# Performance work log

Hardware: AMD Instinct MI355X
Metric: run time of the kernel (lower is better)

The kernel has to match this reference:

```python
import jax, jax.numpy as jnp
import numpy as np

# 5x5 binomial Gaussian kernel, normalized by 256
_K = jnp.array([[1., 4., 6., 4., 1.],
                [4., 16., 24., 16., 4.],
                [6., 24., 36., 24., 6.],
                [4., 16., 24., 16., 4.],
                [1., 4., 6., 4., 1.]], dtype=jnp.float32) / 256.0


def _gauss_conv(img, kernel):
    # depthwise 5x5 conv with reflect padding 2 (same spatial size)
    C = img.shape[1]
    p = jnp.pad(img, ((0, 0), (0, 0), (2, 2), (2, 2)), mode='reflect')
    return jax.lax.conv_general_dilated(
        p, kernel, window_strides=(1, 1), padding='VALID',
        dimension_numbers=('NCHW', 'OIHW', 'NCHW'),
        feature_group_count=C)


def _lap_pyramid(img, kernel, max_levels=5):
    pyr = []
    cur = img
    for _ in range(max_levels):  # fixed small loop over pyramid levels
        H, W = cur.shape[2], cur.shape[3]
        cur = cur[:, :, :H - H % 2, :W - W % 2]  # crop to even size
        down = _gauss_conv(cur, kernel)[:, :, ::2, ::2]
        up = jnp.zeros(cur.shape, cur.dtype).at[:, :, ::2, ::2].set(down * 4.0)
        up = _gauss_conv(up, kernel)
        pyr.append(cur - up)
        cur = down
    return pyr


def setup_inputs() -> dict:
    key = jax.random.key(0)
    k1, k2 = jax.random.split(key)
    predict = jax.random.uniform(k1, (16, 3, 512, 512), dtype=jnp.float32)
    target = jax.random.uniform(k2, (16, 3, 512, 512), dtype=jnp.float32)
    return {"predict": predict, "target": target}


def reference(predict, target):
    C = predict.shape[1]
    kernel = jnp.tile(_K.astype(predict.dtype)[None, None], (C, 1, 1, 1))  # [C,1,5,5]
    pyr_p = _lap_pyramid(predict, kernel, 5)
    pyr_t = _lap_pyramid(target, kernel, 5)
    weights = (1.0, 2.0, 4.0, 8.0, 16.0)
    loss = jnp.asarray(0.0, predict.dtype)
    for w, a, b in zip(weights, pyr_p, pyr_t):
        loss = loss + w * jnp.mean(jnp.abs(a - b))  # F.l1_loss (mean reduction)
    return loss
```

## Files before the change

kernel.cpp:

```cpp
#include <hip/hip_runtime.h>


__device__ __forceinline__ int reflect_i(int m, int S) {
    if (m < 0) m = -m;
    if (m >= S) m = 2 * S - 2 - m;
    return m;
}

__device__ __forceinline__ void wg_barrier() {
    asm volatile("s_waitcnt lgkmcnt(0)" ::: "memory");
    __builtin_amdgcn_s_barrier();
}

#define WAITVM(N) asm volatile("s_waitcnt vmcnt(" #N ")" ::: "memory")
#define WAITLGKM0 asm volatile("s_waitcnt lgkmcnt(0)" ::: "memory")

__device__ __forceinline__ void gld16(const void* g, void* l) {
    __builtin_amdgcn_global_load_lds(
        (const __attribute__((address_space(1))) void*)g,
        (__attribute__((address_space(3))) void*)l, 16, 0, 0);
}

template <int CPL>
__device__ __forceinline__ int swz(int B) {
    if constexpr (CPL == 4) return B ^ (((B >> 7) & 7) << 4);
    else return B;
}

template <int S, int ISL0, int DH>
__global__ __launch_bounds__(64)
void pyr_kernel(const float* __restrict__ a, const float* __restrict__ b,
                float* __restrict__ dwn, float* __restrict__ acc, float scale) {
    constexpr int D = S / 2;
    constexpr int CPL = S / 128;
    constexpr int W = 2 * CPL + 3;
    constexpr int ROWB = (CPL == 1) ? 1024 : S * 4;
    constexpr int NRING = 8;

    __shared__ float4 ringmem[(NRING * ROWB * (ISL0 ? 2 : 1)) / 16];
    char* ra = (char*)ringmem;
    char* rb = ra + NRING * ROWB;

    const int lane = threadIdx.x;
    const int bid = blockIdx.x;
    constexpr int NRS = D / DH;
    const int rs = bid % NRS;
    const int n = bid / NRS;
    const int R0 = rs * DH;
    const size_t gbase = (size_t)n * S * S;

    auto stage_row = [&](int s) {
        int gr = reflect_i(2 * R0 - 4 + s, S);
        const char* ga = (const char*)(a + gbase + (size_t)gr * S);
        char* la = ra + (s & 7) * ROWB;
        if constexpr (CPL == 4) {
            gld16(ga + swz<CPL>(16 * lane), la);
            gld16(ga + swz<CPL>(16 * lane + 1024), la + 1024);
        } else if constexpr (CPL == 2) {
            gld16(ga + 16 * lane, la);
        } else {
            gld16(ga + 16 * (lane & 31), la);
        }
        if constexpr (ISL0) {
            const char* gb = (const char*)(b + gbase + (size_t)gr * S);
            char* lb = rb + (s & 7) * ROWB;
            gld16(gb + swz<CPL>(16 * lane), lb);
            gld16(gb + swz<CPL>(16 * lane + 1024), lb + 1024);
        }
    };

    auto read_win = [&](int s, float* w) {
        const char* pa = ra + (s & 7) * ROWB;
        if constexpr (CPL == 4) {
            int bl = 32 * lane;
            float2 lo = *(const float2*)(pa + swz<CPL>(lane ? bl - 8 : 0));
            float4 m0 = *(const float4*)(pa + swz<CPL>(bl));
            float4 m1 = *(const float4*)(pa + swz<CPL>(bl + 16));
            float hi = *(const float*)(pa + swz<CPL>(lane == 63 ? 2032 : bl + 32));
            w[0]=lo.x; w[1]=lo.y; w[2]=m0.x; w[3]=m0.y; w[4]=m0.z; w[5]=m0.w;
            w[6]=m1.x; w[7]=m1.y; w[8]=m1.z; w[9]=m1.w; w[10]=hi;
            if constexpr (ISL0) {
                const char* pb = rb + (s & 7) * ROWB;
                float2 l2 = *(const float2*)(pb + swz<CPL>(lane ? bl - 8 : 0));
                float4 t0 = *(const float4*)(pb + swz<CPL>(bl));
                float4 t1 = *(const float4*)(pb + swz<CPL>(bl + 16));
                float h2 = *(const float*)(pb + swz<CPL>(lane == 63 ? 2032 : bl + 32));
                w[0]-=l2.x; w[1]-=l2.y; w[2]-=t0.x; w[3]-=t0.y; w[4]-=t0.z;
                w[5]-=t0.w; w[6]-=t1.x; w[7]-=t1.y; w[8]-=t1.z; w[9]-=t1.w; w[10]-=h2;
            }
        } else if constexpr (CPL == 2) {
            int bl = 16 * lane;
            float2 lo = *(const float2*)(pa + (lane ? bl - 8 : 0));
            float4 m0 = *(const float4*)(pa + bl);
            float hi = *(const float*)(pa + (lane == 63 ? 1008 : bl + 16));
            w[0]=lo.x; w[1]=lo.y; w[2]=m0.x; w[3]=m0.y; w[4]=m0.z; w[5]=m0.w; w[6]=hi;
        } else {
            int bl = 8 * lane;
            float2 lo = *(const float2*)(pa + (lane ? bl - 8 : 0));
            float2 m0 = *(const float2*)(pa + bl);
            float hi = *(const float*)(pa + (lane == 63 ? 496 : bl + 8));
            w[0]=lo.x; w[1]=lo.y; w[2]=m0.x; w[3]=m0.y; w[4]=hi;
        }
        if (lane == 0)  { w[0] = w[4]; w[1] = w[3]; }
        if (lane == 63) { w[W - 1] = w[W - 3]; }
    };

    auto read_cur = [&](int s, float* c) {
        const char* pa = ra + (s & 7) * ROWB;
        if constexpr (CPL == 4) {
            int bl = 32 * lane;
            float4 x = *(const float4*)(pa + swz<CPL>(bl));
            float4 y = *(const float4*)(pa + swz<CPL>(bl + 16));
            c[0]=x.x; c[1]=x.y; c[2]=x.z; c[3]=x.w; c[4]=y.x; c[5]=y.y; c[6]=y.z; c[7]=y.w;
            if constexpr (ISL0) {
                const char* pb = rb + (s & 7) * ROWB;
                float4 u = *(const float4*)(pb + swz<CPL>(bl));
                float4 v = *(const float4*)(pb + swz<CPL>(bl + 16));
                c[0]-=u.x; c[1]-=u.y; c[2]-=u.z; c[3]-=u.w;
                c[4]-=v.x; c[5]-=v.y; c[6]-=v.z; c[7]-=v.w;
            }
        } else if constexpr (CPL == 2) {
            float4 x = *(const float4*)(pa + 16 * lane);
            c[0]=x.x; c[1]=x.y; c[2]=x.z; c[3]=x.w;
        } else {
            float2 x = *(const float2*)(pa + 8 * lane);
            c[0]=x.x; c[1]=x.y;
        }
    };

    auto hof = [&](const float* w, float* h) {
        #pragma unroll
        for (int j = 0; j < CPL; j++)
            h[j] = w[2*j] + 4.f*w[2*j+1] + 6.f*w[2*j+2] + 4.f*w[2*j+3] + w[2*j+4];
    };

    #pragma unroll
    for (int s = 0; s < 8; ++s) stage_row(s);
    if constexpr (CPL == 4) { WAITVM(20); } else { WAITVM(5); }

    float hA[CPL], hB[CPL], hC[CPL], hD[CPL], hE[CPL];
    {
        float w[W];
        read_win(0, w); hof(w, hA);
        read_win(1, w); hof(w, hB);
        read_win(2, w); hof(w, hC);
    }
    float ex0[CPL] = {}, ex1[CPL] = {}, ex2[CPL], ox0[CPL] = {}, ox1[CPL] = {}, ox2[CPL];
    float sum = 0.f;
    float* dbase = dwn + (size_t)n * D * D;

    #pragma unroll
    for (int it = 0; it <= DH + 1; ++it) {
        const int m = R0 - 1 + it;
        if (it <= DH) {
            if constexpr (CPL == 4) { WAITVM(12); } else { WAITVM(3); }
        } else {
            WAITVM(0);
        }
        {
            float w[W];
            read_win(2 * it + 3, w); hof(w, hD);
            read_win(2 * it + 4, w); hof(w, hE);
        }
        float d[CPL], dl[CPL], dr[CPL];
        #pragma unroll
        for (int j = 0; j < CPL; j++)
            d[j] = (hA[j] + 4.f*hB[j] + 6.f*hC[j] + 4.f*hD[j] + hE[j]) * (1.f / 256.f);
        float dli = __shfl_up(d[CPL - 1], 1, 64);
        float dri = __shfl_down(d[0], 1, 64);
        dl[0] = (lane == 0) ? ((CPL > 1) ? d[1] : dri) : dli;
        #pragma unroll
        for (int j = 1; j < CPL; j++) dl[j] = d[j - 1];
        dr[CPL - 1] = (lane == 63) ? d[CPL - 1] : dri;
        #pragma unroll
        for (int j = 0; j < CPL - 1; j++) dr[j] = d[j + 1];
        #pragma unroll
        for (int j = 0; j < CPL; j++) {
            ex2[j] = 0.125f * (dl[j] + 6.f * d[j] + dr[j]);
            ox2[j] = 0.5f * (d[j] + dr[j]);
        }

        if (it >= 1 && it <= DH) {
            char* dst = (char*)(dbase + (size_t)m * D + CPL * lane);
            if constexpr (CPL == 4)      *(float4*)dst = make_float4(d[0], d[1], d[2], d[3]);
            else if constexpr (CPL == 2) *(float2*)dst = make_float2(d[0], d[1]);
            else                         *(float*)dst = d[0];
        }

        if (it >= 2) {
            const int me = m - 1;
            float cA[2 * CPL], cB[2 * CPL];
            read_cur(2 * it, cA);
            read_cur(2 * it + 1, cB);
            #pragma unroll
            for (int j = 0; j < CPL; j++) {
                float eA = (me == 0) ? ex2[j] : ex0[j];
                float oA = (me == 0) ? ox2[j] : ox0[j];
                float eC = (me == D - 1) ? ex1[j] : ex2[j];
                float oC = (me == D - 1) ? ox1[j] : ox2[j];
                float uee = 0.125f * (eA + 6.f * ex1[j] + eC);
                float ueo = 0.125f * (oA + 6.f * ox1[j] + oC);
                float uoe = 0.5f * (ex1[j] + eC);
                float uoo = 0.5f * (ox1[j] + oC);
                sum += fabsf(cA[2*j] - uee) + fabsf(cA[2*j+1] - ueo)
                     + fabsf(cB[2*j] - uoe) + fabsf(cB[2*j+1] - uoo);
            }
        }

        #pragma unroll
        for (int j = 0; j < CPL; j++) {
            ex0[j] = ex1[j]; ex1[j] = ex2[j];
            ox0[j] = ox1[j]; ox1[j] = ox2[j];
            hA[j] = hC[j]; hB[j] = hD[j]; hC[j] = hE[j];
        }

        if (it <= DH - 1) {
            WAITLGKM0;
            stage_row(8 + 2 * it);
            stage_row(9 + 2 * it);
        }
    }

    #pragma unroll
    for (int o = 32; o > 0; o >>= 1) sum += __shfl_down(sum, o, 64);
    if (lane == 0) atomicAdd(&acc[bid & 63], sum * scale);
}

__device__ float level_in_lds(const float* cur, float* h, float* dn,
                              int S, int tid, int nt) {
    const int D = S >> 1;
    for (int i = tid; i < S * D; i += nt) {
        int r = i / D, xh = i % D;
        int c0 = reflect_i(2 * xh - 2, S), c1 = reflect_i(2 * xh - 1, S);
        int c3 = 2 * xh + 1, c4 = reflect_i(2 * xh + 2, S);
        const float* row = cur + r * S;
        h[i] = row[c0] + 4.f * row[c1] + 6.f * row[2 * xh] + 4.f * row[c3] + row[c4];
    }
    wg_barrier();
    for (int i = tid; i < D * D; i += nt) {
        int yh = i / D, xh = i % D;
        int r0 = reflect_i(2 * yh - 2, S), r1 = reflect_i(2 * yh - 1, S);
        int r3 = 2 * yh + 1, r4 = reflect_i(2 * yh + 2, S);
        dn[i] = (h[r0 * D + xh] + 4.f * h[r1 * D + xh] + 6.f * h[2 * yh * D + xh]
               + 4.f * h[r3 * D + xh] + h[r4 * D + xh]) * (1.f / 256.f);
    }
    wg_barrier();
    float sum = 0.f;
    for (int i = tid; i < D * D; i += nt) {
        int yh2 = i / D, q = i % D;
        int rm = (yh2 == 0) ? 1 : yh2 - 1;
        int rp = (yh2 == D - 1) ? D - 1 : yh2 + 1;
        int cm = (q == 0) ? 1 : q - 1;
        int cp = (q == D - 1) ? D - 1 : q + 1;
        float A00 = dn[rm * D + cm], A01 = dn[rm * D + q], A02 = dn[rm * D + cp];
        float A10 = dn[yh2 * D + cm], A11 = dn[yh2 * D + q], A12 = dn[yh2 * D + cp];
        float A20 = dn[rp * D + cm], A21 = dn[rp * D + q], A22 = dn[rp * D + cp];
        float ex0 = (A00 + 6.f * A01 + A02) * 0.125f;
        float ex1 = (A10 + 6.f * A11 + A12) * 0.125f;
        float ex2 = (A20 + 6.f * A21 + A22) * 0.125f;
        float ox0 = (A01 + A02) * 0.5f;
        float ox1 = (A11 + A12) * 0.5f;
        float ox2 = (A21 + A22) * 0.5f;
        float uee = (ex0 + 6.f * ex1 + ex2) * 0.125f;
        float ueo = (ox0 + 6.f * ox1 + ox2) * 0.125f;
        float uoe = (ex1 + ex2) * 0.5f;
        float uoo = (ox1 + ox2) * 0.5f;
        const float* c0 = cur + (2 * yh2) * S + 2 * q;
        sum += fabsf(c0[0] - uee) + fabsf(c0[1] - ueo)
             + fabsf(c0[S] - uoe) + fabsf(c0[S + 1] - uoo);
    }
    wg_barrier();
    return sum;
}

__global__ __launch_bounds__(256)
void tail_kernel(const float* __restrict__ d2, float* __restrict__ acc,
                 float s3, float s4) {
    __shared__ float cur[64 * 64];
    __shared__ float hbuf[64 * 32];
    __shared__ float dn3[32 * 32];
    __shared__ float dn4[16 * 16];
    int n = blockIdx.x, tid = threadIdx.x;
    const float4* src = (const float4*)(d2 + (size_t)n * 64 * 64);
    for (int i = tid; i < 64 * 16; i += 256) ((float4*)cur)[i] = src[i];
    wg_barrier();
    float sum = level_in_lds(cur, hbuf, dn3, 64, tid, 256) * s3;
    sum += level_in_lds(dn3, hbuf, dn4, 32, tid, 256) * s4;
    #pragma unroll
    for (int o = 32; o > 0; o >>= 1) sum += __shfl_down(sum, o, 64);
    __shared__ float s[4];
    int lane = tid & 63, w = tid >> 6;
    if (lane == 0) s[w] = sum;
    wg_barrier();
    if (tid == 0) atomicAdd(&acc[n & 63], s[0] + s[1] + s[2] + s[3]);
}

__global__ void finish_kernel(const float* __restrict__ acc, float* __restrict__ out) {
    float v = acc[threadIdx.x];
    #pragma unroll
    for (int o = 32; o > 0; o >>= 1) v += __shfl_down(v, o, 64);
    if (threadIdx.x == 0) out[0] = v;
}

extern "C" void kernel_launch(void* const* d_in, const int* in_sizes, int n_in,
                              void* d_out, int out_size, void* d_ws, size_t ws_size,
                              hipStream_t stream) {
    const float* p = (const float*)d_in[0];
    const float* t = (const float*)d_in[1];
    float* out = (float*)d_out;
    float* acc = (float*)d_ws;
    float* dn0 = acc + 64;
    float* dn1 = dn0 + (size_t)48 * 256 * 256;
    float* dn2 = dn1 + (size_t)48 * 128 * 128;

    hipMemsetAsync(acc, 0, 64 * sizeof(float), stream);

    const int N = 48;

    pyr_kernel<512, 1, 16><<<48 * 16, 64, 0, stream>>>(
        p, t, dn0, acc, 1.f / (float)(N * 512 * 512));
    pyr_kernel<256, 0, 8><<<48 * 16, 64, 0, stream>>>(
        dn0, nullptr, dn1, acc, 2.f / (float)(N * 256 * 256));
    pyr_kernel<128, 0, 4><<<48 * 16, 64, 0, stream>>>(
        dn1, nullptr, dn2, acc, 4.f / (float)(N * 128 * 128));
    tail_kernel<<<N, 256, 0, stream>>>(dn2, acc,
                                       8.f / (float)(N * 64 * 64),
                                       16.f / (float)(N * 32 * 32));
    finish_kernel<<<1, 64, 0, stream>>>(acc, out);
}
```

Baseline: 62.68 us.

## Pack four independent wave strips per block with a smaller LDS ring and register-reused rows

Result: slower. 67.85 us (+8.3%).

```diff
diff --git a/kernel.cpp b/kernel.cpp
--- a/kernel.cpp
+++ b/kernel.cpp
@@ -12,8 +12,16 @@
     __builtin_amdgcn_s_barrier();
 }
 
-#define WAITVM(N) asm volatile("s_waitcnt vmcnt(" #N ")" ::: "memory")
-#define WAITLGKM0 asm volatile("s_waitcnt lgkmcnt(0)" ::: "memory")
+#define LGKM0 asm volatile("s_waitcnt lgkmcnt(0)" ::: "memory")
+
+template <int N>
+__device__ __forceinline__ void wait_vm() {
+    if constexpr (N == 0)      asm volatile("s_waitcnt vmcnt(0)" ::: "memory");
+    else if constexpr (N == 1) asm volatile("s_waitcnt vmcnt(1)" ::: "memory");
+    else if constexpr (N == 2) asm volatile("s_waitcnt vmcnt(2)" ::: "memory");
+    else if constexpr (N == 4) asm volatile("s_waitcnt vmcnt(4)" ::: "memory");
+    else if constexpr (N == 8) asm volatile("s_waitcnt vmcnt(8)" ::: "memory");
+}
 
 __device__ __forceinline__ void gld16(const void* g, void* l) {
     __builtin_amdgcn_global_load_lds(
@@ -21,41 +29,38 @@
         (__attribute__((address_space(3))) void*)l, 16, 0, 0);
 }
 
-template <int CPL>
-__device__ __forceinline__ int swz(int B) {
-    if constexpr (CPL == 4) return B ^ (((B >> 7) & 7) << 4);
-    else return B;
-}
+__device__ __forceinline__ int swz4(int B) { return B ^ (((B >> 7) & 7) << 4); }
 
 template <int S, int ISL0, int DH>
-__global__ __launch_bounds__(64)
+__global__ __launch_bounds__(256, 2)
 void pyr_kernel(const float* __restrict__ a, const float* __restrict__ b,
                 float* __restrict__ dwn, float* __restrict__ acc, float scale) {
     constexpr int D = S / 2;
     constexpr int CPL = S / 128;
     constexpr int W = 2 * CPL + 3;
-    constexpr int ROWB = (CPL == 1) ? 1024 : S * 4;
-    constexpr int NRING = 8;
-
-    __shared__ float4 ringmem[(NRING * ROWB * (ISL0 ? 2 : 1)) / 16];
-    char* ra = (char*)ringmem;
-    char* rb = ra + NRING * ROWB;
-
-    const int lane = threadIdx.x;
-    const int bid = blockIdx.x;
+    constexpr int ROWB = (CPL == 4) ? 2048 : 1024;
+    constexpr int SLOT = ROWB * (ISL0 ? 2 : 1);
+    constexpr int OPS = (CPL == 4) ? (ISL0 ? 4 : 2) : 1;
     constexpr int NRS = D / DH;
-    const int rs = bid % NRS;
-    const int n = bid / NRS;
+
+    __shared__ float4 ringmem[4 * 4 * SLOT / 16];
+    const int wv = threadIdx.x >> 6;
+    const int lane = threadIdx.x & 63;
+    char* ring = (char*)ringmem + wv * (4 * SLOT);
+
+    const int wid = blockIdx.x * 4 + wv;
+    const int rs = wid % NRS;
+    const int n = wid / NRS;
     const int R0 = rs * DH;
     const size_t gbase = (size_t)n * S * S;
 
     auto stage_row = [&](int s) {
         int gr = reflect_i(2 * R0 - 4 + s, S);
         const char* ga = (const char*)(a + gbase + (size_t)gr * S);
-        char* la = ra + (s & 7) * ROWB;
+        char* la = ring + (s & 3) * SLOT;
         if constexpr (CPL == 4) {
-            gld16(ga + swz<CPL>(16 * lane), la);
-            gld16(ga + swz<CPL>(16 * lane + 1024), la + 1024);
+            gld16(ga + swz4(16 * lane), la);
+            gld16(ga + swz4(16 * lane + 1024), la + 1024);
         } else if constexpr (CPL == 2) {
             gld16(ga + 16 * lane, la);
         } else {
@@ -63,28 +68,27 @@
         }
         if constexpr (ISL0) {
             const char* gb = (const char*)(b + gbase + (size_t)gr * S);
-            char* lb = rb + (s & 7) * ROWB;
-            gld16(gb + swz<CPL>(16 * lane), lb);
-            gld16(gb + swz<CPL>(16 * lane + 1024), lb + 1024);
+            gld16(gb + swz4(16 * lane), la + ROWB);
+            gld16(gb + swz4(16 * lane + 1024), la + ROWB + 1024);
         }
     };
 
     auto read_win = [&](int s, float* w) {
-        const char* pa = ra + (s & 7) * ROWB;
+        const char* pa = ring + (s & 3) * SLOT;
         if constexpr (CPL == 4) {
             int bl = 32 * lane;
-            float2 lo = *(const float2*)(pa + swz<CPL>(lane ? bl - 8 : 0));
-            float4 m0 = *(const float4*)(pa + swz<CPL>(bl));
-            float4 m1 = *(const float4*)(pa + swz<CPL>(bl + 16));
-            float hi = *(const float*)(pa + swz<CPL>(lane == 63 ? 2032 : bl + 32));
+            float2 lo = *(const float2*)(pa + swz4(lane ? bl - 8 : 0));
+            float4 m0 = *(const float4*)(pa + swz4(bl));
+            float4 m1 = *(const float4*)(pa + swz4(bl + 16));
+            float hi = *(const float*)(pa + swz4(lane == 63 ? 2032 : bl + 32));
             w[0]=lo.x; w[1]=lo.y; w[2]=m0.x; w[3]=m0.y; w[4]=m0.z; w[5]=m0.w;
             w[6]=m1.x; w[7]=m1.y; w[8]=m1.z; w[9]=m1.w; w[10]=hi;
             if constexpr (ISL0) {
-                const char* pb = rb + (s & 7) * ROWB;
-                float2 l2 = *(const float2*)(pb + swz<CPL>(lane ? bl - 8 : 0));
-                float4 t0 = *(const float4*)(pb + swz<CPL>(bl));
-                float4 t1 = *(const float4*)(pb + swz<CPL>(bl + 16));
-                float h2 = *(const float*)(pb + swz<CPL>(lane == 63 ? 2032 : bl + 32));
+                const char* pb = pa + ROWB;
+                float2 l2 = *(const float2*)(pb + swz4(lane ? bl - 8 : 0));
+                float4 t0 = *(const float4*)(pb + swz4(bl));
+                float4 t1 = *(const float4*)(pb + swz4(bl + 16));
+                float h2 = *(const float*)(pb + swz4(lane == 63 ? 2032 : bl + 32));
                 w[0]-=l2.x; w[1]-=l2.y; w[2]-=t0.x; w[3]-=t0.y; w[4]-=t0.z;
                 w[5]-=t0.w; w[6]-=t1.x; w[7]-=t1.y; w[8]-=t1.z; w[9]-=t1.w; w[10]-=h2;
             }
@@ -105,125 +109,103 @@
         if (lane == 63) { w[W - 1] = w[W - 3]; }
     };
 
-    auto read_cur = [&](int s, float* c) {
-        const char* pa = ra + (s & 7) * ROWB;
-        if constexpr (CPL == 4) {
-            int bl = 32 * lane;
-            float4 x = *(const float4*)(pa + swz<CPL>(bl));
-            float4 y = *(const float4*)(pa + swz<CPL>(bl + 16));
-            c[0]=x.x; c[1]=x.y; c[2]=x.z; c[3]=x.w; c[4]=y.x; c[5]=y.y; c[6]=y.z; c[7]=y.w;
-            if constexpr (ISL0) {
-                const char* pb = rb + (s & 7) * ROWB;
-                float4 u = *(const float4*)(pb + swz<CPL>(bl));
-                float4 v = *(const float4*)(pb + swz<CPL>(bl + 16));
-                c[0]-=u.x; c[1]-=u.y; c[2]-=u.z; c[3]-=u.w;
-                c[4]-=v.x; c[5]-=v.y; c[6]-=v.z; c[7]-=v.w;
-            }
-        } else if constexpr (CPL == 2) {
-            float4 x = *(const float4*)(pa + 16 * lane);
-            c[0]=x.x; c[1]=x.y; c[2]=x.z; c[3]=x.w;
-        } else {
-            float2 x = *(const float2*)(pa + 8 * lane);
-            c[0]=x.x; c[1]=x.y;
-        }
-    };
-
     auto hof = [&](const float* w, float* h) {
         #pragma unroll
         for (int j = 0; j < CPL; j++)
             h[j] = w[2*j] + 4.f*w[2*j+1] + 6.f*w[2*j+2] + 4.f*w[2*j+3] + w[2*j+4];
     };
 
-    #pragma unroll
-    for (int s = 0; s < 8; ++s) stage_row(s);
-    if constexpr (CPL == 4) { WAITVM(20); } else { WAITVM(5); }
-
     float hA[CPL], hB[CPL], hC[CPL], hD[CPL], hE[CPL];
+    float cEv1[2*CPL], cEv2[2*CPL], cOd1[2*CPL];
+    float ex0[CPL] = {}, ex1[CPL] = {}, ox0[CPL] = {}, ox1[CPL] = {};
+    float sum = 0.f;
+    float* dbase = dwn + (size_t)n * D * D;
+
+    stage_row(0); stage_row(1); stage_row(2); stage_row(3);
+    wait_vm<OPS>();
     {
         float w[W];
         read_win(0, w); hof(w, hA);
         read_win(1, w); hof(w, hB);
         read_win(2, w); hof(w, hC);
     }
-    float ex0[CPL] = {}, ex1[CPL] = {}, ex2[CPL], ox0[CPL] = {}, ox1[CPL] = {}, ox2[CPL];
-    float sum = 0.f;
-    float* dbase = dwn + (size_t)n * D * D;
+    LGKM0;
+    stage_row(4); stage_row(5); stage_row(6);
 
     #pragma unroll
-    for (int it = 0; it <= DH + 1; ++it) {
-        const int m = R0 - 1 + it;
-        if (it <= DH) {
-            if constexpr (CPL == 4) { WAITVM(12); } else { WAITVM(3); }
-        } else {
-            WAITVM(0);
-        }
-        {
-            float w[W];
-            read_win(2 * it + 3, w); hof(w, hD);
-            read_win(2 * it + 4, w); hof(w, hE);
-        }
-        float d[CPL], dl[CPL], dr[CPL];
-        #pragma unroll
-        for (int j = 0; j < CPL; j++)
-            d[j] = (hA[j] + 4.f*hB[j] + 6.f*hC[j] + 4.f*hD[j] + hE[j]) * (1.f / 256.f);
+    for (int j = 0; j <= DH + 1; ++j) {
+        const int m = R0 - 1 + j;
+        if (j <= DH) wait_vm<2 * OPS>(); else wait_vm<0>();
+
+        float w3[W], w4[W];
+        read_win(2 * j + 3, w3); hof(w3, hD);
+        read_win(2 * j + 4, w4); hof(w4, hE);
+
+        float d[CPL], dl[CPL], dr[CPL], ex2[CPL], ox2[CPL];
+        #pragma unroll
+        for (int q = 0; q < CPL; q++)
+            d[q] = (hA[q] + 4.f*hB[q] + 6.f*hC[q] + 4.f*hD[q] + hE[q]) * (1.f / 256.f);
         float dli = __shfl_up(d[CPL - 1], 1, 64);
         float dri = __shfl_down(d[0], 1, 64);
         dl[0] = (lane == 0) ? ((CPL > 1) ? d[1] : dri) : dli;
         #pragma unroll
-        for (int j = 1; j < CPL; j++) dl[j] = d[j - 1];
+        for (int q = 1; q < CPL; q++) dl[q] = d[q - 1];
         dr[CPL - 1] = (lane == 63) ? d[CPL - 1] : dri;
         #pragma unroll
-        for (int j = 0; j < CPL - 1; j++) dr[j] = d[j + 1];
-        #pragma unroll
-        for (int j = 0; j < CPL; j++) {
-            ex2[j] = 0.125f * (dl[j] + 6.f * d[j] + dr[j]);
-            ox2[j] = 0.5f * (d[j] + dr[j]);
-        }
-
-        if (it >= 1 && it <= DH) {
+        for (int q = 0; q < CPL - 1; q++) dr[q] = d[q + 1];
+        #pragma unroll
+        for (int q = 0; q < CPL; q++) {
+            ex2[q] = 0.125f * (dl[q] + 6.f * d[q] + dr[q]);
+            ox2[q] = 0.5f * (d[q] + dr[q]);
+        }
+
+        if (j >= 1 && j <= DH) {
             char* dst = (char*)(dbase + (size_t)m * D + CPL * lane);
             if constexpr (CPL == 4)      *(float4*)dst = make_float4(d[0], d[1], d[2], d[3]);
             else if constexpr (CPL == 2) *(float2*)dst = make_float2(d[0], d[1]);
             else                         *(float*)dst = d[0];
         }
 
-        if (it >= 2) {
+        if (j >= 2) {
             const int me = m - 1;
-            float cA[2 * CPL], cB[2 * CPL];
-            read_cur(2 * it, cA);
-            read_cur(2 * it + 1, cB);
             #pragma unroll
-            for (int j = 0; j < CPL; j++) {
-                float eA = (me == 0) ? ex2[j] : ex0[j];
-                float oA = (me == 0) ? ox2[j] : ox0[j];
-                float eC = (me == D - 1) ? ex1[j] : ex2[j];
-                float oC = (me == D - 1) ? ox1[j] : ox2[j];
-                float uee = 0.125f * (eA + 6.f * ex1[j] + eC);
-                float ueo = 0.125f * (oA + 6.f * ox1[j] + oC);
-                float uoe = 0.5f * (ex1[j] + eC);
-                float uoo = 0.5f * (ox1[j] + oC);
-                sum += fabsf(cA[2*j] - uee) + fabsf(cA[2*j+1] - ueo)
-                     + fabsf(cB[2*j] - uoe) + fabsf(cB[2*j+1] - uoo);
+            for (int q = 0; q < CPL; q++) {
+                float eA = (me == 0) ? ex2[q] : ex0[q];
+                float oA = (me == 0) ? ox2[q] : ox0[q];
+                float eC = (me == D - 1) ? ex1[q] : ex2[q];
+                float oC = (me == D - 1) ? ox1[q] : ox2[q];
+                float uee = 0.125f * (eA + 6.f * ex1[q] + eC);
+                float ueo = 0.125f * (oA + 6.f * ox1[q] + oC);
+                float uoe = 0.5f * (ex1[q] + eC);
+                float uoo = 0.5f * (ox1[q] + oC);
+                sum += fabsf(cEv2[2*q]   - uee) + fabsf(cEv2[2*q+1] - ueo)
+                     + fabsf(cOd1[2*q]   - uoe) + fabsf(cOd1[2*q+1] - uoo);
             }
         }
 
         #pragma unroll
-        for (int j = 0; j < CPL; j++) {
-            ex0[j] = ex1[j]; ex1[j] = ex2[j];
-            ox0[j] = ox1[j]; ox1[j] = ox2[j];
-            hA[j] = hC[j]; hB[j] = hD[j]; hC[j] = hE[j];
-        }
-
-        if (it <= DH - 1) {
-            WAITLGKM0;
-            stage_row(8 + 2 * it);
-            stage_row(9 + 2 * it);
+        for (int q = 0; q < CPL; q++) {
+            ex0[q] = ex1[q]; ex1[q] = ex2[q];
+            ox0[q] = ox1[q]; ox1[q] = ox2[q];
+            hA[q] = hC[q]; hB[q] = hD[q]; hC[q] = hE[q];
+        }
+        #pragma unroll
+        for (int q = 0; q < 2 * CPL; q++) {
+            cEv2[q] = cEv1[q];
+            cEv1[q] = w4[2 + q];
+            cOd1[q] = w3[2 + q];
+        }
+
+        if (j <= DH - 1) {
+            LGKM0;
+            stage_row(2 * j + 7);
+            stage_row(2 * j + 8);
         }
     }
 
     #pragma unroll
     for (int o = 32; o > 0; o >>= 1) sum += __shfl_down(sum, o, 64);
-    if (lane == 0) atomicAdd(&acc[bid & 63], sum * scale);
+    if (lane == 0) atomicAdd(&acc[wid & 63], sum * scale);
 }
 
 __device__ float level_in_lds(const float* cur, float* h, float* dn,
@@ -317,11 +299,11 @@
 
     const int N = 48;
 
-    pyr_kernel<512, 1, 16><<<48 * 16, 64, 0, stream>>>(
+    pyr_kernel<512, 1, 8><<<384, 256, 0, stream>>>(
         p, t, dn0, acc, 1.f / (float)(N * 512 * 512));
-    pyr_kernel<256, 0, 8><<<48 * 16, 64, 0, stream>>>(
+    pyr_kernel<256, 0, 4><<<384, 256, 0, stream>>>(
         dn0, nullptr, dn1, acc, 2.f / (float)(N * 256 * 256));
-    pyr_kernel<128, 0, 4><<<48 * 16, 64, 0, stream>>>(
+    pyr_kernel<128, 0, 4><<<192, 256, 0, stream>>>(
         dn1, nullptr, dn2, acc, 4.f / (float)(N * 128 * 128));
     tail_kernel<<<N, 256, 0, stream>>>(dn2, acc,
                                        8.f / (float)(N * 64 * 64),
```
